# Performance work log

Measured on AMD Instinct MI355X. Metric: run time of the kernel, lower is better.

Reference implementation:

```python
import jax, jax.numpy as jnp
import numpy as np


def setup_inputs() -> dict:
    key = jax.random.key(0)
    k1, k2, k3 = jax.random.split(key, 3)
    B, C, D, H, W = 4, 64, 32, 64, 64
    K = 32
    X = jax.random.normal(k1, (B, C, D, H, W), dtype=jnp.float32)
    std1 = 1.0 / float(np.sqrt(K * C))
    codewords = jax.random.uniform(k2, (K, C), minval=-std1, maxval=std1, dtype=jnp.float32)
    scale = jax.random.uniform(k3, (K,), minval=-1.0, maxval=0.0, dtype=jnp.float32)
    return {"X": X, "codewords": codewords, "scale": scale}


def reference(X, codewords, scale):
    B, C, D, H, W = X.shape
    K = codewords.shape[0]
    N = D * H * W
    # (B, N, C) feature view
    Xf = jnp.transpose(X.reshape(B, C, N), (0, 2, 1))
    X2 = jnp.sum(Xf * Xf, axis=-1, keepdims=True)          # (B, N, 1)
    C2 = jnp.sum(codewords * codewords, axis=-1)            # (K,)
    XC = jnp.einsum('bnc,kc->bnk', Xf, codewords)           # (B, N, K)
    logits = scale * (X2 + C2 - 2.0 * XC)
    A = jax.nn.softmax(logits, axis=2)                      # (B, N, K)
    # coefA: (B, K, D, H, W); dropout is identity in eval mode
    coefA = jnp.transpose(A, (0, 2, 1)).reshape(B, K, D, H, W)
    # aggregate: E[b,k,:] = sum_n A[b,n,k]*(X[b,n,:]-C[k,:])
    # algebraic rewrite: A^T @ X - (sum_n A) * C   (avoids (B,N,K,C) blowup)
    AtX = jnp.einsum('bnk,bnc->bkc', A, Xf)                 # (B, K, C)
    Asum = jnp.sum(A, axis=1)                               # (B, K)
    E = AtX - Asum[..., None] * codewords[None, :, :]
    return (E, coefA)
```

## Files before the change

### kernel.cpp

```cpp
#include <hip/hip_runtime.h>
#include <hip/hip_bf16.h>

typedef short short8 __attribute__((ext_vector_type(8)));
typedef float f32x4  __attribute__((ext_vector_type(4)));

#define BB      4
#define CC      64
#define KK      32
#define NN      131072
#define TILE    128
#define NTILE   1024
#define JBLK    192
#define THREADS 256
#define PSZ     2080

#define WS_SC2 (768 * PSZ)
#define WS_S2  (WS_SC2 + 32)
#define WS_SCL (WS_S2 + 32)

#define XN_S 72
#define XC_S 136
#define AK_S 136

__device__ __forceinline__ unsigned pk2(float a, float b) {
    union { __hip_bfloat162 h; unsigned u; } cv;
    cv.h = __float22bfloat162_rn(make_float2(a, b));
    return cv.u;
}
__device__ __forceinline__ unsigned short b16(float a) {
    union { __hip_bfloat16 h; unsigned short u; } cv;
    cv.h = __float2bfloat16(a);
    return cv.u;
}

__global__ void precompute_kernel(const float* __restrict__ cw,
                                  const float* __restrict__ scale,
                                  float* __restrict__ ws) {
    int k = threadIdx.x;
    if (k < KK) {
        float c2 = 0.f;
        #pragma unroll
        for (int c = 0; c < CC; ++c) { float v = cw[k * CC + c]; c2 += v * v; }
        ws[WS_SC2 + k] = scale[k] * c2;
        ws[WS_S2  + k] = -2.0f * scale[k];
        ws[WS_SCL + k] = scale[k];
    }
}

__global__ __launch_bounds__(THREADS, 3) void main_kernel(
        const float* __restrict__ X,
        const float* __restrict__ cw,
        float* __restrict__ out,
        float* __restrict__ ws) {
    __shared__ __align__(16) unsigned short Xn[TILE][XN_S];
    __shared__ __align__(16) unsigned short Xc[CC][XC_S];
    __shared__ __align__(16) unsigned short Ak[KK][AK_S];
    __shared__ float x2l[2][TILE];
    __shared__ float asml[4][KK];

    const int tid  = threadIdx.x;
    const int b    = blockIdx.x / JBLK;
    const int j    = blockIdx.x % JBLK;
    const int lane = tid & 63;
    const int w    = tid >> 6;
    const int q    = lane >> 4;
    const int l15  = lane & 15;

    const float* Xb   = X + (size_t)b * CC * NN;
    float*       outA = out + 8192 + (size_t)b * KK * NN;

    short8 cwf[2][2];
    #pragma unroll
    for (int kt = 0; kt < 2; ++kt)
        #pragma unroll
        for (int s = 0; s < 2; ++s) {
            const float* cp = cw + (16 * kt + l15) * CC + 32 * s + 8 * q;
            #pragma unroll
            for (int jj = 0; jj < 8; ++jj) cwf[kt][s][jj] = (short)b16(cp[jj]);
        }
    float s2v[2][4], sc2v[2][4], sclv[2][4];
    #pragma unroll
    for (int t2 = 0; t2 < 2; ++t2)
        #pragma unroll
        for (int r = 0; r < 4; ++r) {
            int k = 16 * t2 + 4 * q + r;
            s2v[t2][r]  = ws[WS_S2 + k];
            sc2v[t2][r] = ws[WS_SC2 + k];
            sclv[t2][r] = ws[WS_SCL + k];
        }

    const f32x4 zf = {0.f, 0.f, 0.f, 0.f};
    f32x4 acc2[2] = {zf, zf};
    float asum[2][4];
    #pragma unroll
    for (int t2 = 0; t2 < 2; ++t2)
        #pragma unroll
        for (int r = 0; r < 4; ++r) asum[t2][r] = 0.f;

    const int n1 = tid & 127, ch = tid >> 7;
    const int c2i = tid >> 2, ng = tid & 3;
    const int kt2 = w & 1, ct0 = (w >> 1) * 2;

    for (int t = j; t < NTILE; t += JBLK) {
        const size_t nb = (size_t)t * TILE;

        float xv[32];
        const float* p1 = Xb + (size_t)(32 * ch) * NN + nb + n1;
        #pragma unroll
        for (int i = 0; i < 32; ++i) xv[i] = p1[(size_t)i * NN];
        float yv[32];
        const float* p2 = Xb + (size_t)c2i * NN + nb + 32 * ng;
        #pragma unroll
        for (int i = 0; i < 32; ++i) yv[i] = p2[i];

        float x2 = 0.f;
        #pragma unroll
        for (int i = 0; i < 32; ++i) x2 += xv[i] * xv[i];
        x2l[ch][n1] = x2;
        #pragma unroll
        for (int g = 0; g < 4; ++g) {
            uint4 u;
            u.x = pk2(xv[8*g+0], xv[8*g+1]); u.y = pk2(xv[8*g+2], xv[8*g+3]);
            u.z = pk2(xv[8*g+4], xv[8*g+5]); u.w = pk2(xv[8*g+6], xv[8*g+7]);
            *(uint4*)&Xn[n1][32 * ch + 8 * g] = u;
        }
        #pragma unroll
        for (int g = 0; g < 4; ++g) {
            uint4 u;
            u.x = pk2(yv[8*g+0], yv[8*g+1]); u.y = pk2(yv[8*g+2], yv[8*g+3]);
            u.z = pk2(yv[8*g+4], yv[8*g+5]); u.w = pk2(yv[8*g+6], yv[8*g+7]);
            *(uint4*)&Xc[c2i][32 * ng + 8 * g] = u;
        }
        __syncthreads();

        #pragma unroll
        for (int nt = 2 * w; nt < 2 * w + 2; ++nt) {
            const int nl = nt * 16 + l15;
            const float x2n = x2l[0][nl] + x2l[1][nl];
            short8 bx0 = *(const short8*)&Xn[nl][8 * q];
            short8 bx1 = *(const short8*)&Xn[nl][32 + 8 * q];
            f32x4 lt[2];
            lt[0] = __builtin_amdgcn_mfma_f32_16x16x32_bf16(cwf[0][0], bx0, zf, 0, 0, 0);
            lt[0] = __builtin_amdgcn_mfma_f32_16x16x32_bf16(cwf[0][1], bx1, lt[0], 0, 0, 0);
            lt[1] = __builtin_amdgcn_mfma_f32_16x16x32_bf16(cwf[1][0], bx0, zf, 0, 0, 0);
            lt[1] = __builtin_amdgcn_mfma_f32_16x16x32_bf16(cwf[1][1], bx1, lt[1], 0, 0, 0);

            float av[2][4];
            float m = -3.0e38f;
            #pragma unroll
            for (int t2 = 0; t2 < 2; ++t2)
                #pragma unroll
                for (int r = 0; r < 4; ++r) {
                    float L = fmaf(s2v[t2][r], lt[t2][r],
                                   fmaf(sclv[t2][r], x2n, sc2v[t2][r]));
                    av[t2][r] = L;
                    m = fmaxf(m, L);
                }
            m = fmaxf(m, __shfl_xor(m, 16));
            m = fmaxf(m, __shfl_xor(m, 32));
            float s = 0.f;
            #pragma unroll
            for (int t2 = 0; t2 < 2; ++t2)
                #pragma unroll
                for (int r = 0; r < 4; ++r) {
                    float e = __expf(av[t2][r] - m);
                    av[t2][r] = e;
                    s += e;
                }
            s += __shfl_xor(s, 16);
            s += __shfl_xor(s, 32);
            const float inv = 1.0f / s;
            #pragma unroll
            for (int t2 = 0; t2 < 2; ++t2)
                #pragma unroll
                for (int r = 0; r < 4; ++r) {
                    float a = av[t2][r] * inv;
                    int k = 16 * t2 + 4 * q + r;
                    asum[t2][r] += a;
                    outA[(size_t)k * NN + nb + nl] = a;
                    Ak[k][nl] = b16(a);
                }
        }
        __syncthreads();

        #pragma unroll
        for (int s = 0; s < 4; ++s) {
            short8 af  = *(const short8*)&Ak[16 * kt2 + l15][32 * s + 8 * q];
            short8 bc0 = *(const short8*)&Xc[16 * ct0 + l15][32 * s + 8 * q];
            short8 bc1 = *(const short8*)&Xc[16 * (ct0 + 1) + l15][32 * s + 8 * q];
            acc2[0] = __builtin_amdgcn_mfma_f32_16x16x32_bf16(af, bc0, acc2[0], 0, 0, 0);
            acc2[1] = __builtin_amdgcn_mfma_f32_16x16x32_bf16(af, bc1, acc2[1], 0, 0, 0);
        }
        __syncthreads();
    }

    float* p = ws + (size_t)blockIdx.x * PSZ;
    #pragma unroll
    for (int cti = 0; cti < 2; ++cti)
        #pragma unroll
        for (int r = 0; r < 4; ++r) {
            int k = 16 * kt2 + 4 * q + r;
            int c = 16 * (ct0 + cti) + l15;
            p[k * CC + c] = acc2[cti][r];
        }
    #pragma unroll
    for (int t2 = 0; t2 < 2; ++t2)
        #pragma unroll
        for (int r = 0; r < 4; ++r) {
            float v = asum[t2][r];
            v += __shfl_xor(v, 1); v += __shfl_xor(v, 2);
            v += __shfl_xor(v, 4); v += __shfl_xor(v, 8);
            if (l15 == 0) asml[w][16 * t2 + 4 * q + r] = v;
        }
    __syncthreads();
    if (tid < KK)
        p[2048 + tid] = asml[0][tid] + asml[1][tid] + asml[2][tid] + asml[3][tid];
}

__global__ __launch_bounds__(256) void finalize_kernel(
        const float* __restrict__ cw,
        float* __restrict__ out,
        const float* __restrict__ ws) {
    __shared__ float red[4][64];
    __shared__ float ar[192];
    const int b = blockIdx.x >> 5;
    const int k = blockIdx.x & 31;
    const int c  = threadIdx.x & 63;
    const int jg = threadIdx.x >> 6;

    const float* p0 = ws + (size_t)b * JBLK * PSZ;
    float atx = 0.f;
    for (int j2 = jg; j2 < JBLK; j2 += 4)
        atx += p0[(size_t)j2 * PSZ + k * CC + c];
    red[jg][c] = atx;
    if (threadIdx.x < 192)
        ar[threadIdx.x] = p0[(size_t)threadIdx.x * PSZ + 2048 + k];
    __syncthreads();
    if (threadIdx.x < 64) {
        float a = red[0][c] + red[1][c] + red[2][c] + red[3][c];
        float s = ar[c] + ar[c + 64] + ar[c + 128];
        s += __shfl_xor(s, 1);  s += __shfl_xor(s, 2);  s += __shfl_xor(s, 4);
        s += __shfl_xor(s, 8);  s += __shfl_xor(s, 16); s += __shfl_xor(s, 32);
        out[(size_t)(b * KK + k) * CC + c] = a - s * cw[k * CC + c];
    }
}

extern "C" void kernel_launch(void* const* d_in, const int* in_sizes, int n_in,
                              void* d_out, int out_size, void* d_ws, size_t ws_size,
                              hipStream_t stream) {
    const float* X  = (const float*)d_in[0];
    const float* cw = (const float*)d_in[1];
    const float* sc = (const float*)d_in[2];
    float* out = (float*)d_out;
    float* ws  = (float*)d_ws;

    precompute_kernel<<<1, 64, 0, stream>>>(cw, sc, ws);
    main_kernel<<<BB * JBLK, THREADS, 0, stream>>>(X, cw, out, ws);
    finalize_kernel<<<BB * KK, 256, 0, stream>>>(cw, out, ws);
}
```

Measured before the change: 257.9 us.

## Prefetch next X tile into registers, drop duplicate X load and precompute kernel

Removes the separate precompute kernel and computes codeword norms and scale terms inside main_kernel with wave shuffles. The second, row-major global read of X is dropped, and the channel-major Xc tile is built from the same registers via scalar LDS stores. The next tile's X is loaded into registers right after the first barrier so the global loads overlap the softmax and MFMA work. __syncthreads is replaced with an LDS-only waitcnt plus s_barrier, so the prefetched global loads are not drained at each barrier. The cost is 32 extra live registers per thread under a 3-blocks-per-SM launch bound, which risks spills, plus more LDS store instructions for the transposed Xc writes.

```diff
diff --git a/kernel.cpp b/kernel.cpp
--- a/kernel.cpp
+++ b/kernel.cpp
@@ -14,13 +14,14 @@
 #define THREADS 256
 #define PSZ     2080
 
-#define WS_SC2 (768 * PSZ)
-#define WS_S2  (WS_SC2 + 32)
-#define WS_SCL (WS_S2 + 32)
-
 #define XN_S 72
 #define XC_S 136
 #define AK_S 136
+
+__device__ __forceinline__ void barrier_lds() {
+    __builtin_amdgcn_s_waitcnt(0xC07F);
+    __builtin_amdgcn_s_barrier();
+}
 
 __device__ __forceinline__ unsigned pk2(float a, float b) {
     union { __hip_bfloat162 h; unsigned u; } cv;
@@ -33,23 +34,10 @@
     return cv.u;
 }
 
-__global__ void precompute_kernel(const float* __restrict__ cw,
-                                  const float* __restrict__ scale,
-                                  float* __restrict__ ws) {
-    int k = threadIdx.x;
-    if (k < KK) {
-        float c2 = 0.f;
-        #pragma unroll
-        for (int c = 0; c < CC; ++c) { float v = cw[k * CC + c]; c2 += v * v; }
-        ws[WS_SC2 + k] = scale[k] * c2;
-        ws[WS_S2  + k] = -2.0f * scale[k];
-        ws[WS_SCL + k] = scale[k];
-    }
-}
-
 __global__ __launch_bounds__(THREADS, 3) void main_kernel(
         const float* __restrict__ X,
         const float* __restrict__ cw,
+        const float* __restrict__ scale,
         float* __restrict__ out,
         float* __restrict__ ws) {
     __shared__ __align__(16) unsigned short Xn[TILE][XN_S];
@@ -70,23 +58,35 @@
     float*       outA = out + 8192 + (size_t)b * KK * NN;
 
     short8 cwf[2][2];
+    float c2acc[2] = {0.f, 0.f};
     #pragma unroll
     for (int kt = 0; kt < 2; ++kt)
         #pragma unroll
         for (int s = 0; s < 2; ++s) {
             const float* cp = cw + (16 * kt + l15) * CC + 32 * s + 8 * q;
             #pragma unroll
-            for (int jj = 0; jj < 8; ++jj) cwf[kt][s][jj] = (short)b16(cp[jj]);
-        }
+            for (int jj = 0; jj < 8; ++jj) {
+                float v = cp[jj];
+                c2acc[kt] += v * v;
+                cwf[kt][s][jj] = (short)b16(v);
+            }
+        }
+    #pragma unroll
+    for (int kt = 0; kt < 2; ++kt) {
+        c2acc[kt] += __shfl_xor(c2acc[kt], 16);
+        c2acc[kt] += __shfl_xor(c2acc[kt], 32);
+    }
     float s2v[2][4], sc2v[2][4], sclv[2][4];
     #pragma unroll
     for (int t2 = 0; t2 < 2; ++t2)
         #pragma unroll
         for (int r = 0; r < 4; ++r) {
             int k = 16 * t2 + 4 * q + r;
-            s2v[t2][r]  = ws[WS_S2 + k];
-            sc2v[t2][r] = ws[WS_SC2 + k];
-            sclv[t2][r] = ws[WS_SCL + k];
+            float sk  = scale[k];
+            float c2k = __shfl(c2acc[t2], 4 * q + r);
+            sclv[t2][r] = sk;
+            s2v[t2][r]  = -2.0f * sk;
+            sc2v[t2][r] = sk * c2k;
         }
 
     const f32x4 zf = {0.f, 0.f, 0.f, 0.f};
@@ -98,20 +98,17 @@
         for (int r = 0; r < 4; ++r) asum[t2][r] = 0.f;
 
     const int n1 = tid & 127, ch = tid >> 7;
-    const int c2i = tid >> 2, ng = tid & 3;
     const int kt2 = w & 1, ct0 = (w >> 1) * 2;
+
+    float xv[32];
+    {
+        const float* p1 = Xb + (size_t)(32 * ch) * NN + (size_t)j * TILE + n1;
+        #pragma unroll
+        for (int i = 0; i < 32; ++i) xv[i] = p1[(size_t)i * NN];
+    }
 
     for (int t = j; t < NTILE; t += JBLK) {
         const size_t nb = (size_t)t * TILE;
-
-        float xv[32];
-        const float* p1 = Xb + (size_t)(32 * ch) * NN + nb + n1;
-        #pragma unroll
-        for (int i = 0; i < 32; ++i) xv[i] = p1[(size_t)i * NN];
-        float yv[32];
-        const float* p2 = Xb + (size_t)c2i * NN + nb + 32 * ng;
-        #pragma unroll
-        for (int i = 0; i < 32; ++i) yv[i] = p2[i];
 
         float x2 = 0.f;
         #pragma unroll
@@ -125,13 +122,18 @@
             *(uint4*)&Xn[n1][32 * ch + 8 * g] = u;
         }
         #pragma unroll
-        for (int g = 0; g < 4; ++g) {
-            uint4 u;
-            u.x = pk2(yv[8*g+0], yv[8*g+1]); u.y = pk2(yv[8*g+2], yv[8*g+3]);
-            u.z = pk2(yv[8*g+4], yv[8*g+5]); u.w = pk2(yv[8*g+6], yv[8*g+7]);
-            *(uint4*)&Xc[c2i][32 * ng + 8 * g] = u;
-        }
-        __syncthreads();
+        for (int i = 0; i < 32; ++i)
+            Xc[32 * ch + i][n1] = b16(xv[i]);
+
+        barrier_lds();
+
+        const int tn = t + JBLK;
+        float xn[32];
+        if (tn < NTILE) {
+            const float* pn = Xb + (size_t)(32 * ch) * NN + (size_t)tn * TILE + n1;
+            #pragma unroll
+            for (int i = 0; i < 32; ++i) xn[i] = pn[(size_t)i * NN];
+        }
 
         #pragma unroll
         for (int nt = 2 * w; nt < 2 * w + 2; ++nt) {
@@ -181,7 +183,8 @@
                     Ak[k][nl] = b16(a);
                 }
         }
-        __syncthreads();
+
+        barrier_lds();
 
         #pragma unroll
         for (int s = 0; s < 4; ++s) {
@@ -191,7 +194,13 @@
             acc2[0] = __builtin_amdgcn_mfma_f32_16x16x32_bf16(af, bc0, acc2[0], 0, 0, 0);
             acc2[1] = __builtin_amdgcn_mfma_f32_16x16x32_bf16(af, bc1, acc2[1], 0, 0, 0);
         }
-        __syncthreads();
+
+        barrier_lds();
+
+        if (tn < NTILE) {
+            #pragma unroll
+            for (int i = 0; i < 32; ++i) xv[i] = xn[i];
+        }
     }
 
     float* p = ws + (size_t)blockIdx.x * PSZ;
@@ -212,7 +221,7 @@
             v += __shfl_xor(v, 4); v += __shfl_xor(v, 8);
             if (l15 == 0) asml[w][16 * t2 + 4 * q + r] = v;
         }
-    __syncthreads();
+    barrier_lds();
     if (tid < KK)
         p[2048 + tid] = asml[0][tid] + asml[1][tid] + asml[2][tid] + asml[3][tid];
 }
@@ -254,7 +263,6 @@
     float* out = (float*)d_out;
     float* ws  = (float*)d_ws;
 
-    precompute_kernel<<<1, 64, 0, stream>>>(cw, sc, ws);
-    main_kernel<<<BB * JBLK, THREADS, 0, stream>>>(X, cw, out, ws);
+    main_kernel<<<BB * JBLK, THREADS, 0, stream>>>(X, cw, sc, out, ws);
     finalize_kernel<<<BB * KK, 256, 0, stream>>>(cw, out, ws);
 }
```

After: 238.9 us. -7.4%, faster.
